# Kernel optimization log

Measured on AMD Instinct MI355X. Metric: run time of the kernel, lower is better.

Reference implementation:

```python
import jax, jax.numpy as jnp
import numpy as np

HOP = jnp.array([0, 1, 4, 7, 2, 5, 8, 3, 6, 9, 11, 14, 10, 12, 15, 13, 16])
GRAPH = jnp.array([0, 1, 4, 7, 2, 5, 8, 3, 6, 9, 12, 10, 13, 15, 11, 14, 16])
D_MODEL, L, D_INNER, D_STATE, DT_RANK = 512, 17, 1024, 4, 32


def layernorm(x, w, b, eps=1e-5):
    mu = x.mean(-1, keepdims=True)
    var = ((x - mu) ** 2).mean(-1, keepdims=True)
    return (x - mu) * jax.lax.rsqrt(var + eps) * w + b


def setup_inputs() -> dict:
    key = jax.random.key(0)
    ks = jax.random.split(key, 9)
    B = 4096
    s = lambda k, shape: jax.random.normal(k, shape, jnp.float32) * 0.02
    # A_log init per mamba_ssm: log(1..d_state) repeated over d_inner
    A_log = jnp.log(jnp.broadcast_to(jnp.arange(1, D_STATE + 1, dtype=jnp.float32), (D_INNER, D_STATE)))
    return {
        "x": jax.random.normal(ks[0], (B, L, D_MODEL), jnp.float32),
        "bp_embed": s(ks[1], (1, 5, D_MODEL)),
        "ln_w": jnp.ones((D_MODEL,), jnp.float32),
        "ln_b": jnp.zeros((D_MODEL,), jnp.float32),
        "in_proj_w": s(ks[2], (2 * D_INNER, D_MODEL)),
        "conv_w": 1.0 + s(ks[3], (D_INNER,)),  # d_conv=1 depthwise conv == per-channel scale
        "conv_b": jnp.zeros((D_INNER,), jnp.float32),
        "x_proj_w": s(ks[4], (DT_RANK + 2 * D_STATE, D_INNER)),
        "dt_proj_w": s(ks[5], (D_INNER, DT_RANK)),
        "dt_proj_b": s(ks[6], (D_INNER,)) - 4.0,  # softplus-inverse-ish small dt init
        "A_log": A_log,
        "D": jnp.ones((D_INNER,), jnp.float32),
        "out_proj_w": s(ks[7], (D_MODEL, D_INNER)),
    }


def mamba(u, in_proj_w, conv_w, conv_b, x_proj_w, dt_proj_w, dt_proj_b, A_log, D, out_proj_w):
    # u: [B, L, d_model]
    xz = jnp.einsum('bld,ed->ble', u, in_proj_w)          # [B,L,2*d_inner]
    xm, z = jnp.split(xz, 2, axis=-1)
    xm = jax.nn.silu(xm * conv_w + conv_b)                 # d_conv=1 -> pointwise
    x_dbl = jnp.einsum('ble,fe->blf', xm, x_proj_w)        # [B,L,dt_rank+2*d_state]
    dt_r = x_dbl[..., :DT_RANK]
    Bm = x_dbl[..., DT_RANK:DT_RANK + D_STATE]
    Cm = x_dbl[..., DT_RANK + D_STATE:]
    dt = jax.nn.softplus(jnp.einsum('blr,er->ble', dt_r, dt_proj_w) + dt_proj_b)  # [B,L,d_inner]
    A = -jnp.exp(A_log)                                    # [d_inner,d_state]

    def step(h, inp):
        dt_t, B_t, C_t, x_t = inp                          # [B,di],[B,ds],[B,ds],[B,di]
        dA = jnp.exp(dt_t[..., None] * A)                  # [B,di,ds]
        h = dA * h + (dt_t * x_t)[..., None] * B_t[:, None, :]
        y = jnp.einsum('bes,bs->be', h, C_t)
        return h, y

    bsz = u.shape[0]
    h0 = jnp.zeros((bsz, D_INNER, D_STATE), u.dtype)
    seq = (dt.transpose(1, 0, 2), Bm.transpose(1, 0, 2), Cm.transpose(1, 0, 2), xm.transpose(1, 0, 2))
    _, ys = jax.lax.scan(step, h0, seq)                    # ys: [L,B,d_inner]
    y = ys.transpose(1, 0, 2) + xm * D
    y = y * jax.nn.silu(z)
    return jnp.einsum('ble,de->bld', y, out_proj_w)


def reference(x, bp_embed, ln_w, ln_b, in_proj_w, conv_w, conv_b, x_proj_w,
              dt_proj_w, dt_proj_b, A_log, D, out_proj_w):
    bp = bp_embed
    x_bpe = jnp.concatenate([bp[:, :3], bp[:, :3], bp[:, :3], bp[:, :1],
                             bp[:, 3:], bp[:, :1], bp[:, 3:], bp[:, 3:]], axis=1)  # [1,17,dim]
    x_ssm = x[:, HOP, :] + x_bpe
    x_ssm = layernorm(x_ssm, ln_w, ln_b)
    x_ssm = mamba(x_ssm, in_proj_w, conv_w, conv_b, x_proj_w,
                  dt_proj_w, dt_proj_b, A_log, D, out_proj_w)
    return x + x_ssm[:, GRAPH, :]
```

## Files before the change

### kernel.cpp

```cpp
#include <hip/hip_runtime.h>

typedef unsigned short u16;
typedef unsigned int   u32;
typedef __bf16 bf16_t;
typedef bf16_t bf16x8 __attribute__((ext_vector_type(8)));
typedef float  f32x4  __attribute__((ext_vector_type(4)));

#define DEV static __device__ __forceinline__

__constant__ int c_HOP[17] = {0,1,4,7,2,5,8,3,6,9,11,14,10,12,15,13,16};
__constant__ int c_BPE[17] = {0,1,2,0,1,2,0,1,2,0,3,4,0,3,4,3,4};

DEV u16 f2bf(float f){
  u32 x = __builtin_bit_cast(u32, f);
  x += 0x7fffu + ((x >> 16) & 1u);
  return (u16)(x >> 16);
}
DEV float bf2f(u32 u){ return __builtin_bit_cast(float, u << 16); }
DEV float silu_f(float v){ return v / (1.f + __expf(-v)); }
DEV float softplus_f(float s){ return (s > 20.f) ? s : log1pf(__expf(s)); }

DEV void gll16(const void* g, void* l){
  __builtin_amdgcn_global_load_lds((__attribute__((address_space(1))) void*)g,
                                   (__attribute__((address_space(3))) void*)l,
                                   16, 0, 0);
}

__global__ __launch_bounds__(256) void cvt4(
    const float* __restrict__ s0, u16* __restrict__ d0, int n0,
    const float* __restrict__ s1, u16* __restrict__ d1, int n1,
    const float* __restrict__ s2, u16* __restrict__ d2, int n2,
    const float* __restrict__ s3, u16* __restrict__ d3, int n3)
{
  int t = blockIdx.x * 256 + threadIdx.x;
  if (t < n0){ d0[t] = f2bf(s0[t]); return; }
  t -= n0; if (t < n1){ d1[t] = f2bf(s1[t]); return; }
  t -= n1; if (t < n2){ d2[t] = f2bf(s2[t]); return; }
  t -= n2; if (t < n3){ d3[t] = f2bf(s3[t]); }
}

__global__ __launch_bounds__(256) void ln_gather(
    const float* __restrict__ x, const float* __restrict__ bpe,
    const float* __restrict__ lnw, const float* __restrict__ lnb,
    u16* __restrict__ u)
{
  int tok = blockIdx.x;
  int b = tok / 17;
  int l = tok - b * 17;
  const float* xr = x   + ((size_t)b * 17 + c_HOP[l]) * 512;
  const float* br = bpe + (size_t)c_BPE[l] * 512;
  int tid = threadIdx.x;
  int d0 = tid * 2;
  float2 xv = *(const float2*)(xr + d0);
  float2 bv = *(const float2*)(br + d0);
  float v0 = xv.x + bv.x, v1 = xv.y + bv.y;

  __shared__ float red[8];
  float s = v0 + v1;
  #pragma unroll
  for (int o = 32; o; o >>= 1) s += __shfl_xor(s, o);
  if ((tid & 63) == 0) red[tid >> 6] = s;
  __syncthreads();
  float mu = (red[0] + red[1] + red[2] + red[3]) * (1.f / 512.f);
  float a0 = v0 - mu, a1 = v1 - mu;
  float q = a0 * a0 + a1 * a1;
  #pragma unroll
  for (int o = 32; o; o >>= 1) q += __shfl_xor(q, o);
  if ((tid & 63) == 0) red[4 + (tid >> 6)] = q;
  __syncthreads();
  float var = (red[4] + red[5] + red[6] + red[7]) * (1.f / 512.f);
  float rs = rsqrtf(var + 1e-5f);

  u16 o0 = f2bf(a0 * rs * lnw[d0]     + lnb[d0]);
  u16 o1 = f2bf(a1 * rs * lnw[d0 + 1] + lnb[d0 + 1]);
  u32 pack = (u32)o0 | ((u32)o1 << 16);
  *(u32*)(u + (size_t)tok * 512 + d0) = pack;
}

enum { EPI_SPLIT = 0, EPI_OUT = 1, EPI_XDBL = 2, EPI_DT = 3 };

template<int EPI>
__global__ __launch_bounds__(512, 2) void gemm256(
    const u16* __restrict__ A, int lda,
    const u16* __restrict__ W, int K, int MT,
    u16* __restrict__ ob0, u16* __restrict__ ob1,
    const float* __restrict__ p0, const float* __restrict__ p1,
    const float* __restrict__ xres, float* __restrict__ fout)
{
  __shared__ u16 sA[2][2][8192];
  __shared__ u16 sB[2][2][8192];

  int nwg = gridDim.x;
  int cpx = nwg >> 3;
  int wg = (blockIdx.x & 7) * cpx + (blockIdx.x >> 3);
  int NT = nwg / MT;
  int nt = wg % NT, mt = wg / NT;
  int brow = mt * 256, bcol = nt * 256;
  int tid = threadIdx.x, lane = tid & 63, wid = tid >> 6;
  int wm = wid >> 2, wn = wid & 3;
  int l15 = lane & 15, lhi = lane >> 4;

  f32x4 acc[8][4] = {};

  int sr0 = tid >> 2, sr1 = 128 + (tid >> 2), sch = tid & 3;
  const u16* gA0 = A + (size_t)(brow + sr0) * lda + (sch ^ ((sr0 >> 1) & 3)) * 8;
  const u16* gA1 = A + (size_t)(brow + sr1) * lda + (sch ^ ((sr1 >> 1) & 3)) * 8;
  const u16* gW0 = W + (size_t)(bcol + sr0) * K   + (sch ^ ((sr0 >> 1) & 3)) * 8;
  const u16* gW1 = W + (size_t)(bcol + sr1) * K   + (sch ^ ((sr1 >> 1) & 3)) * 8;

  auto stA = [&](int buf, int kh, int koff) {
    char* d = (char*)&sA[buf][kh][0] + tid * 16;
    gll16(gA0 + koff, d);
    gll16(gA1 + koff, d + 8192);
  };
  auto stB = [&](int buf, int kh, int koff) {
    char* d = (char*)&sB[buf][kh][0] + tid * 16;
    gll16(gW0 + koff, d);
    gll16(gW1 + koff, d + 8192);
  };

  int aoff[2][4], boff[4];
  #pragma unroll
  for (int mh = 0; mh < 2; mh++)
    #pragma unroll
    for (int mi = 0; mi < 4; mi++) {
      int r = wm * 128 + mh * 64 + mi * 16 + l15;
      aoff[mh][mi] = r * 64 + ((lhi ^ ((r >> 1) & 3)) * 16);
    }
  #pragma unroll
  for (int ni = 0; ni < 4; ni++) {
    int r = wn * 64 + ni * 16 + l15;
    boff[ni] = r * 64 + ((lhi ^ ((r >> 1) & 3)) * 16);
  }

  bf16x8 bvv[4];

#define PH(buf, kh, MH, RB, STAGE)                                          \
  {                                                                         \
    const char* la = (const char*)&sA[buf][kh][0];                          \
    bf16x8 av0 = *(const bf16x8*)(la + aoff[MH][0]);                        \
    bf16x8 av1 = *(const bf16x8*)(la + aoff[MH][1]);                        \
    bf16x8 av2 = *(const bf16x8*)(la + aoff[MH][2]);                        \
    bf16x8 av3 = *(const bf16x8*)(la + aoff[MH][3]);                        \
    if (RB) {                                                               \
      const char* lb = (const char*)&sB[buf][kh][0];                        \
      bvv[0] = *(const bf16x8*)(lb + boff[0]);                              \
      bvv[1] = *(const bf16x8*)(lb + boff[1]);                              \
      bvv[2] = *(const bf16x8*)(lb + boff[2]);                              \
      bvv[3] = *(const bf16x8*)(lb + boff[3]);                              \
    }                                                                       \
    STAGE                                                                   \
    __builtin_amdgcn_s_barrier();                                           \
    __builtin_amdgcn_sched_barrier(0);                                      \
    __builtin_amdgcn_s_setprio(1);                                          \
    _Pragma("unroll")                                                       \
    for (int ni = 0; ni < 4; ni++) {                                        \
      acc[(MH)*4+0][ni] = __builtin_amdgcn_mfma_f32_16x16x32_bf16(av0, bvv[ni], acc[(MH)*4+0][ni], 0,0,0); \
      acc[(MH)*4+1][ni] = __builtin_amdgcn_mfma_f32_16x16x32_bf16(av1, bvv[ni], acc[(MH)*4+1][ni], 0,0,0); \
      acc[(MH)*4+2][ni] = __builtin_amdgcn_mfma_f32_16x16x32_bf16(av2, bvv[ni], acc[(MH)*4+2][ni], 0,0,0); \
      acc[(MH)*4+3][ni] = __builtin_amdgcn_mfma_f32_16x16x32_bf16(av3, bvv[ni], acc[(MH)*4+3][ni], 0,0,0); \
    }                                                                       \
    __builtin_amdgcn_s_setprio(0);                                          \
  }

  int T = K >> 6;

  stA(0, 0, 0);  stB(0, 0, 0);
  stA(0, 1, 32); stB(0, 1, 32);
  stA(1, 0, 64); stB(1, 0, 64);
  asm volatile("s_waitcnt vmcnt(8)" ::: "memory");
  __builtin_amdgcn_s_barrier();

  for (int t = 0; t < T; ++t) {
    int b = t & 1;
    bool s1 = (t + 1 < T), s2 = (t + 2 < T);
    int k1off = ((t + 1) << 6) + 32;
    int k2off = (t + 2) << 6;

    PH(b, 0, 0, true,  { if (s1) stA(b ^ 1, 1, k1off); });
    __builtin_amdgcn_s_barrier();
    PH(b, 0, 1, false, { if (s1) stB(b ^ 1, 1, k1off); });
    if (t < T - 1) { asm volatile("s_waitcnt vmcnt(8)" ::: "memory"); }
    else           { asm volatile("s_waitcnt vmcnt(0)" ::: "memory"); }
    __builtin_amdgcn_s_barrier();
    PH(b, 1, 0, true,  { if (s2) stA(b, 0, k2off); });
    __builtin_amdgcn_s_barrier();
    PH(b, 1, 1, false, { if (s2) stB(b, 0, k2off); });
    if (t < T - 2)       { asm volatile("s_waitcnt vmcnt(8)" ::: "memory"); }
    else if (t == T - 2) { asm volatile("s_waitcnt vmcnt(4)" ::: "memory"); }
    __builtin_amdgcn_s_barrier();
  }
#undef PH

  int r4 = lhi * 4;
  #pragma unroll
  for (int fm = 0; fm < 8; fm++) {
    int rowb = brow + wm * 128 + fm * 16 + r4;
    #pragma unroll
    for (int ni = 0; ni < 4; ni++) {
      int col = bcol + wn * 64 + ni * 16 + l15;
      if constexpr (EPI == EPI_SPLIT) {
        bool isx = (bcol < 1024);
        int cidx = isx ? col : 0;
        float cw = isx ? p0[cidx] : 1.f;
        float cb = isx ? p1[cidx] : 0.f;
        u16* dst = isx ? (ob0 + col) : (ob1 + col - 1024);
        #pragma unroll
        for (int rr = 0; rr < 4; rr++)
          dst[(size_t)(rowb + rr) * 1024] = f2bf(silu_f(acc[fm][ni][rr] * cw + cb));
      } else {
        #pragma unroll
        for (int rr = 0; rr < 4; rr++) {
          int row = rowb + rr;
          u32 rw = (u32)row;
          u32 b = rw / 17u;
          int gl = (int)(rw - b * 17u);
          size_t oi = ((size_t)b * 17 + c_HOP[gl]) * 512 + col;
          fout[oi] = xres[oi] + acc[fm][ni][rr];
        }
      }
    }
  }
}

template<int EPI>
__global__ __launch_bounds__(256) void gemm_bt(
    const u16* __restrict__ A, int lda,
    const u16* __restrict__ W, int K, int MT,
    u16* __restrict__ ob0, const float* __restrict__ p0)
{
  __shared__ u16 sA[2][128 * 32];
  __shared__ u16 sW[2][128 * 32];
  int nwg = gridDim.x;
  int cpx = nwg >> 3;
  int wg = (blockIdx.x & 7) * cpx + (blockIdx.x >> 3);
  int NT = nwg / MT;
  int nt = wg % NT, mt = wg / NT;
  int brow = mt * 128, bcol = nt * 128;
  int tid = threadIdx.x, lane = tid & 63, wid = tid >> 6;
  int wm = wid >> 1, wn = wid & 1;

  f32x4 acc[4][4] = {};

  int srow = tid >> 2;
  int sch  = tid & 3;

  const u16* gA0 = A + (size_t)(brow + srow)      * lda + (sch ^ ((srow >> 1) & 3)) * 8;
  const u16* gA1 = A + (size_t)(brow + 64 + srow) * lda + (sch ^ (((64 + srow) >> 1) & 3)) * 8;
  const u16* gW0 = W + (size_t)(bcol + srow)      * K   + (sch ^ ((srow >> 1) & 3)) * 8;
  const u16* gW1 = W + (size_t)(bcol + 64 + srow) * K   + (sch ^ (((64 + srow) >> 1) & 3)) * 8;

  auto STAGE = [&](int buf, int kt) {
    gll16(gA0 + kt, (char*)sA[buf] + tid * 16);
    gll16(gA1 + kt, (char*)sA[buf] + tid * 16 + 4096);
    gll16(gW0 + kt, (char*)sW[buf] + tid * 16);
    gll16(gW1 + kt, (char*)sW[buf] + tid * 16 + 4096);
  };

  int aoff[4], boff[4];
  #pragma unroll
  for (int mi = 0; mi < 4; mi++) {
    int r = wm * 64 + mi * 16 + (lane & 15);
    aoff[mi] = r * 64 + (((lane >> 4) ^ ((r >> 1) & 3)) * 16);
  }
  #pragma unroll
  for (int ni = 0; ni < 4; ni++) {
    int r = wn * 64 + ni * 16 + (lane & 15);
    boff[ni] = r * 64 + (((lane >> 4) ^ ((r >> 1) & 3)) * 16);
  }

  auto COMPUTE = [&](int buf) {
    bf16x8 av[4], bv[4];
    #pragma unroll
    for (int mi = 0; mi < 4; mi++)
      av[mi] = *(const bf16x8*)((const char*)sA[buf] + aoff[mi]);
    #pragma unroll
    for (int ni = 0; ni < 4; ni++)
      bv[ni] = *(const bf16x8*)((const char*)sW[buf] + boff[ni]);
    #pragma unroll
    for (int mi = 0; mi < 4; mi++)
      #pragma unroll
      for (int ni = 0; ni < 4; ni++)
        acc[mi][ni] = __builtin_amdgcn_mfma_f32_16x16x32_bf16(
            av[mi], bv[ni], acc[mi][ni], 0, 0, 0);
  };

  int nsteps = K >> 5;
  STAGE(0, 0);
  __syncthreads();
  int cur = 0;
  for (int s = 1; s < nsteps; ++s) {
    STAGE(cur ^ 1, s << 5);
    COMPUTE(cur);
    __syncthreads();
    cur ^= 1;
  }
  COMPUTE(cur);

  int r4 = (lane >> 4) * 4;
  int cl = lane & 15;
  #pragma unroll
  for (int mi = 0; mi < 4; mi++) {
    int rowb = brow + wm * 64 + mi * 16 + r4;
    #pragma unroll
    for (int ni = 0; ni < 4; ni++) {
      int col = bcol + wn * 64 + ni * 16 + cl;
      if constexpr (EPI == EPI_XDBL) {
        if (col < 40) {
          #pragma unroll
          for (int rr = 0; rr < 4; rr++)
            ob0[(size_t)(rowb + rr) * 40 + col] = f2bf(acc[mi][ni][rr]);
        }
      } else {
        float bb = p0[col];
        #pragma unroll
        for (int rr = 0; rr < 4; rr++)
          ob0[(size_t)(rowb + rr) * 1024 + col] = f2bf(softplus_f(acc[mi][ni][rr] + bb));
      }
    }
  }
}

__global__ __launch_bounds__(128) void scan5(
    const u16* __restrict__ xm, const u16* __restrict__ zs,
    const u16* __restrict__ xdbl, u16* __restrict__ dty,
    const float* __restrict__ A_log, const float* __restrict__ Dp)
{
  int b = blockIdx.x;
  int tid = threadIdx.x;
  int e0 = tid * 8;
  const size_t base = (size_t)b * 17 * 1024;

  float4 al = *(const float4*)(A_log + (size_t)e0 * 4);
  float A0 = -__expf(al.x), A1 = -__expf(al.y);
  float A2 = -__expf(al.z), A3 = -__expf(al.w);
  float Dv[8];
  *(float4*)(Dv)     = *(const float4*)(Dp + e0);
  *(float4*)(Dv + 4) = *(const float4*)(Dp + e0 + 4);

  const u16* xmb = xm + base + e0;
  const u16* zsb = zs + base + e0;
  u16* db = dty + base + e0;
  const u16* bcb = xdbl + (size_t)b * 680 + 32;

  float h[8][4];
  #pragma unroll
  for (int c = 0; c < 8; c++)
    #pragma unroll
    for (int s = 0; s < 4; s++) h[c][s] = 0.f;

  #pragma unroll
  for (int t = 0; t < 17; t++) {
    uint4 xr = *(const uint4*)(xmb + t * 1024);
    uint4 zr = *(const uint4*)(zsb + t * 1024);
    uint4 dr = *(const uint4*)(db + t * 1024);
    uint4 bc = *(const uint4*)(bcb + t * 40);
    float B0 = bf2f(bc.x & 0xffffu), B1 = bf2f(bc.x >> 16);
    float B2 = bf2f(bc.y & 0xffffu), B3 = bf2f(bc.y >> 16);
    float C0 = bf2f(bc.z & 0xffffu), C1 = bf2f(bc.z >> 16);
    float C2 = bf2f(bc.w & 0xffffu), C3 = bf2f(bc.w >> 16);
    u32 yo[4];
    const u32* xw = (const u32*)&xr;
    const u32* zw = (const u32*)&zr;
    const u32* dw = (const u32*)&dr;
    #pragma unroll
    for (int c = 0; c < 8; c++) {
      u32 x16 = (c & 1) ? (xw[c >> 1] >> 16) : (xw[c >> 1] & 0xffffu);
      u32 z16 = (c & 1) ? (zw[c >> 1] >> 16) : (zw[c >> 1] & 0xffffu);
      u32 d16 = (c & 1) ? (dw[c >> 1] >> 16) : (dw[c >> 1] & 0xffffu);
      float xv = bf2f(x16), zv = bf2f(z16), dtv = bf2f(d16);
      float dx = dtv * xv;
      h[c][0] = __expf(dtv * A0) * h[c][0] + dx * B0;
      h[c][1] = __expf(dtv * A1) * h[c][1] + dx * B1;
      h[c][2] = __expf(dtv * A2) * h[c][2] + dx * B2;
      h[c][3] = __expf(dtv * A3) * h[c][3] + dx * B3;
      float yv = h[c][0] * C0 + h[c][1] * C1 + h[c][2] * C2 + h[c][3] * C3;
      u16 pk = f2bf((yv + xv * Dv[c]) * zv);
      if (c & 1) yo[c >> 1] |= ((u32)pk << 16);
      else       yo[c >> 1] = (u32)pk;
    }
    *(uint4*)(db + t * 1024) = *(uint4*)yo;
  }
}

extern "C" void kernel_launch(void* const* d_in, const int* in_sizes, int n_in,
                              void* d_out, int out_size, void* d_ws, size_t ws_size,
                              hipStream_t stream) {
  const float* x     = (const float*)d_in[0];
  const float* bpe   = (const float*)d_in[1];
  const float* lnw   = (const float*)d_in[2];
  const float* lnb   = (const float*)d_in[3];
  const float* w_in  = (const float*)d_in[4];
  const float* convw = (const float*)d_in[5];
  const float* convb = (const float*)d_in[6];
  const float* w_xp  = (const float*)d_in[7];
  const float* w_dt  = (const float*)d_in[8];
  const float* b_dt  = (const float*)d_in[9];
  const float* A_log = (const float*)d_in[10];
  const float* Dp    = (const float*)d_in[11];
  const float* w_out = (const float*)d_in[12];
  float* out = (float*)d_out;

  u16* ws = (u16*)d_ws;
  u16* wb_in  = ws;
  u16* wb_out = wb_in  + 1048576;
  u16* wb_xp  = wb_out + 524288;
  u16* wb_dt  = wb_xp  + 40960;
  u16* xm     = wb_dt  + 32768;
  u16* zs     = xm     + 71303168;
  u16* xdbl   = zs     + 71303168;
  u16* dty    = xdbl   + 2785280;
  u16* u      = dty;

  const int MT2 = 272;
  const int MT1 = 544;

  cvt4<<<6432, 256, 0, stream>>>(w_in, wb_in, 1048576, w_out, wb_out, 524288,
                                 w_xp, wb_xp, 40960, w_dt, wb_dt, 32768);

  ln_gather<<<69632, 256, 0, stream>>>(x, bpe, lnw, lnb, u);

  gemm256<EPI_SPLIT><<<MT2 * 8, 512, 0, stream>>>(
      u, 512, wb_in, 512, MT2, xm, zs, convw, convb, nullptr, nullptr);

  gemm_bt<EPI_XDBL><<<MT1 * 1, 256, 0, stream>>>(
      xm, 1024, wb_xp, 1024, MT1, xdbl, nullptr);

  gemm_bt<EPI_DT><<<MT1 * 8, 256, 0, stream>>>(
      xdbl, 40, wb_dt, 32, MT1, dty, b_dt);

  scan5<<<4096, 128, 0, stream>>>(xm, zs, xdbl, dty, A_log, Dp);

  gemm256<EPI_OUT><<<MT2 * 2, 512, 0, stream>>>(
      dty, 1024, wb_out, 1024, MT2, nullptr, nullptr, nullptr, nullptr, x, out);
}
```

Measured before the change: 872.0 us.

## Fuse x_proj and dt_proj GEMMs into one kernel and restructure gemm256 main loop

Merges the x_proj GEMM and the dt_proj GEMM with softplus into a single kernel. The 32-wide dt_rank slice stays in shared memory and feeds a second small MFMA stage, so there is no separate launch and no global round trip for that slice. Separately, the gemm256 inner loop now issues the A and B loads for each half-step together, then runs 32 MFMAs per half in place of four phases with extra barriers. The x_proj weight rows are clamped to row 39 to avoid out-of-bounds reads, which adds some redundant staging. The fused kernel's dt epilogue has only 544 blocks doing scattered 2-byte stores, which could limit parallelism.

```diff
diff --git a/kernel.cpp b/kernel.cpp
--- a/kernel.cpp
+++ b/kernel.cpp
@@ -77,7 +77,7 @@
   *(u32*)(u + (size_t)tok * 512 + d0) = pack;
 }
 
-enum { EPI_SPLIT = 0, EPI_OUT = 1, EPI_XDBL = 2, EPI_DT = 3 };
+enum { EPI_SPLIT = 0, EPI_OUT = 1 };
 
 template<int EPI>
 __global__ __launch_bounds__(512, 2) void gemm256(
@@ -133,34 +133,56 @@
     boff[ni] = r * 64 + ((lhi ^ ((r >> 1) & 3)) * 16);
   }
 
-  bf16x8 bvv[4];
-
-#define PH(buf, kh, MH, RB, STAGE)                                          \
-  {                                                                         \
-    const char* la = (const char*)&sA[buf][kh][0];                          \
-    bf16x8 av0 = *(const bf16x8*)(la + aoff[MH][0]);                        \
-    bf16x8 av1 = *(const bf16x8*)(la + aoff[MH][1]);                        \
-    bf16x8 av2 = *(const bf16x8*)(la + aoff[MH][2]);                        \
-    bf16x8 av3 = *(const bf16x8*)(la + aoff[MH][3]);                        \
-    if (RB) {                                                               \
-      const char* lb = (const char*)&sB[buf][kh][0];                        \
-      bvv[0] = *(const bf16x8*)(lb + boff[0]);                              \
-      bvv[1] = *(const bf16x8*)(lb + boff[1]);                              \
-      bvv[2] = *(const bf16x8*)(lb + boff[2]);                              \
-      bvv[3] = *(const bf16x8*)(lb + boff[3]);                              \
-    }                                                                       \
-    STAGE                                                                   \
-    __builtin_amdgcn_s_barrier();                                           \
-    __builtin_amdgcn_sched_barrier(0);                                      \
-    __builtin_amdgcn_s_setprio(1);                                          \
-    _Pragma("unroll")                                                       \
-    for (int ni = 0; ni < 4; ni++) {                                        \
-      acc[(MH)*4+0][ni] = __builtin_amdgcn_mfma_f32_16x16x32_bf16(av0, bvv[ni], acc[(MH)*4+0][ni], 0,0,0); \
-      acc[(MH)*4+1][ni] = __builtin_amdgcn_mfma_f32_16x16x32_bf16(av1, bvv[ni], acc[(MH)*4+1][ni], 0,0,0); \
-      acc[(MH)*4+2][ni] = __builtin_amdgcn_mfma_f32_16x16x32_bf16(av2, bvv[ni], acc[(MH)*4+2][ni], 0,0,0); \
-      acc[(MH)*4+3][ni] = __builtin_amdgcn_mfma_f32_16x16x32_bf16(av3, bvv[ni], acc[(MH)*4+3][ni], 0,0,0); \
-    }                                                                       \
-    __builtin_amdgcn_s_setprio(0);                                          \
+#define HALF(BUF, KH)                                                        \
+  {                                                                          \
+    const char* la = (const char*)&sA[BUF][KH][0];                           \
+    const char* lb = (const char*)&sB[BUF][KH][0];                           \
+    bf16x8 bv0 = *(const bf16x8*)(lb + boff[0]);                             \
+    bf16x8 bv1 = *(const bf16x8*)(lb + boff[1]);                             \
+    bf16x8 bv2 = *(const bf16x8*)(lb + boff[2]);                             \
+    bf16x8 bv3 = *(const bf16x8*)(lb + boff[3]);                             \
+    bf16x8 a0 = *(const bf16x8*)(la + aoff[0][0]);                           \
+    bf16x8 a1 = *(const bf16x8*)(la + aoff[0][1]);                           \
+    bf16x8 a2 = *(const bf16x8*)(la + aoff[0][2]);                           \
+    bf16x8 a3 = *(const bf16x8*)(la + aoff[0][3]);                           \
+    __builtin_amdgcn_s_setprio(1);                                           \
+    acc[0][0] = __builtin_amdgcn_mfma_f32_16x16x32_bf16(a0, bv0, acc[0][0],0,0,0); \
+    acc[1][0] = __builtin_amdgcn_mfma_f32_16x16x32_bf16(a1, bv0, acc[1][0],0,0,0); \
+    acc[2][0] = __builtin_amdgcn_mfma_f32_16x16x32_bf16(a2, bv0, acc[2][0],0,0,0); \
+    acc[3][0] = __builtin_amdgcn_mfma_f32_16x16x32_bf16(a3, bv0, acc[3][0],0,0,0); \
+    acc[0][1] = __builtin_amdgcn_mfma_f32_16x16x32_bf16(a0, bv1, acc[0][1],0,0,0); \
+    acc[1][1] = __builtin_amdgcn_mfma_f32_16x16x32_bf16(a1, bv1, acc[1][1],0,0,0); \
+    acc[2][1] = __builtin_amdgcn_mfma_f32_16x16x32_bf16(a2, bv1, acc[2][1],0,0,0); \
+    acc[3][1] = __builtin_amdgcn_mfma_f32_16x16x32_bf16(a3, bv1, acc[3][1],0,0,0); \
+    acc[0][2] = __builtin_amdgcn_mfma_f32_16x16x32_bf16(a0, bv2, acc[0][2],0,0,0); \
+    acc[1][2] = __builtin_amdgcn_mfma_f32_16x16x32_bf16(a1, bv2, acc[1][2],0,0,0); \
+    acc[2][2] = __builtin_amdgcn_mfma_f32_16x16x32_bf16(a2, bv2, acc[2][2],0,0,0); \
+    acc[3][2] = __builtin_amdgcn_mfma_f32_16x16x32_bf16(a3, bv2, acc[3][2],0,0,0); \
+    acc[0][3] = __builtin_amdgcn_mfma_f32_16x16x32_bf16(a0, bv3, acc[0][3],0,0,0); \
+    acc[1][3] = __builtin_amdgcn_mfma_f32_16x16x32_bf16(a1, bv3, acc[1][3],0,0,0); \
+    acc[2][3] = __builtin_amdgcn_mfma_f32_16x16x32_bf16(a2, bv3, acc[2][3],0,0,0); \
+    acc[3][3] = __builtin_amdgcn_mfma_f32_16x16x32_bf16(a3, bv3, acc[3][3],0,0,0); \
+    a0 = *(const bf16x8*)(la + aoff[1][0]);                                  \
+    a1 = *(const bf16x8*)(la + aoff[1][1]);                                  \
+    a2 = *(const bf16x8*)(la + aoff[1][2]);                                  \
+    a3 = *(const bf16x8*)(la + aoff[1][3]);                                  \
+    acc[4][0] = __builtin_amdgcn_mfma_f32_16x16x32_bf16(a0, bv0, acc[4][0],0,0,0); \
+    acc[5][0] = __builtin_amdgcn_mfma_f32_16x16x32_bf16(a1, bv0, acc[5][0],0,0,0); \
+    acc[6][0] = __builtin_amdgcn_mfma_f32_16x16x32_bf16(a2, bv0, acc[6][0],0,0,0); \
+    acc[7][0] = __builtin_amdgcn_mfma_f32_16x16x32_bf16(a3, bv0, acc[7][0],0,0,0); \
+    acc[4][1] = __builtin_amdgcn_mfma_f32_16x16x32_bf16(a0, bv1, acc[4][1],0,0,0); \
+    acc[5][1] = __builtin_amdgcn_mfma_f32_16x16x32_bf16(a1, bv1, acc[5][1],0,0,0); \
+    acc[6][1] = __builtin_amdgcn_mfma_f32_16x16x32_bf16(a2, bv1, acc[6][1],0,0,0); \
+    acc[7][1] = __builtin_amdgcn_mfma_f32_16x16x32_bf16(a3, bv1, acc[7][1],0,0,0); \
+    acc[4][2] = __builtin_amdgcn_mfma_f32_16x16x32_bf16(a0, bv2, acc[4][2],0,0,0); \
+    acc[5][2] = __builtin_amdgcn_mfma_f32_16x16x32_bf16(a1, bv2, acc[5][2],0,0,0); \
+    acc[6][2] = __builtin_amdgcn_mfma_f32_16x16x32_bf16(a2, bv2, acc[6][2],0,0,0); \
+    acc[7][2] = __builtin_amdgcn_mfma_f32_16x16x32_bf16(a3, bv2, acc[7][2],0,0,0); \
+    acc[4][3] = __builtin_amdgcn_mfma_f32_16x16x32_bf16(a0, bv3, acc[4][3],0,0,0); \
+    acc[5][3] = __builtin_amdgcn_mfma_f32_16x16x32_bf16(a1, bv3, acc[5][3],0,0,0); \
+    acc[6][3] = __builtin_amdgcn_mfma_f32_16x16x32_bf16(a2, bv3, acc[6][3],0,0,0); \
+    acc[7][3] = __builtin_amdgcn_mfma_f32_16x16x32_bf16(a3, bv3, acc[7][3],0,0,0); \
+    __builtin_amdgcn_s_setprio(0);                                           \
   }
 
   int T = K >> 6;
@@ -170,27 +192,25 @@
   stA(1, 0, 64); stB(1, 0, 64);
   asm volatile("s_waitcnt vmcnt(8)" ::: "memory");
   __builtin_amdgcn_s_barrier();
+  __builtin_amdgcn_sched_barrier(0);
 
   for (int t = 0; t < T; ++t) {
-    int b = t & 1;
-    bool s1 = (t + 1 < T), s2 = (t + 2 < T);
-    int k1off = ((t + 1) << 6) + 32;
-    int k2off = (t + 2) << 6;
-
-    PH(b, 0, 0, true,  { if (s1) stA(b ^ 1, 1, k1off); });
-    __builtin_amdgcn_s_barrier();
-    PH(b, 0, 1, false, { if (s1) stB(b ^ 1, 1, k1off); });
+    int bb_ = t & 1;
+    if (t + 1 < T) { int ko = ((t + 1) << 6) + 32; stA(bb_ ^ 1, 1, ko); stB(bb_ ^ 1, 1, ko); }
+    HALF(bb_, 0);
     if (t < T - 1) { asm volatile("s_waitcnt vmcnt(8)" ::: "memory"); }
     else           { asm volatile("s_waitcnt vmcnt(0)" ::: "memory"); }
     __builtin_amdgcn_s_barrier();
-    PH(b, 1, 0, true,  { if (s2) stA(b, 0, k2off); });
+    __builtin_amdgcn_sched_barrier(0);
+    if (t + 2 < T) { int ko = (t + 2) << 6; stA(bb_, 0, ko); stB(bb_, 0, ko); }
+    HALF(bb_, 1);
+    if (t < T - 2)      { asm volatile("s_waitcnt vmcnt(8)" ::: "memory"); }
+    else if (t == T - 2){ asm volatile("s_waitcnt vmcnt(4)" ::: "memory"); }
+    else                { asm volatile("s_waitcnt vmcnt(0)" ::: "memory"); }
     __builtin_amdgcn_s_barrier();
-    PH(b, 1, 1, false, { if (s2) stB(b, 0, k2off); });
-    if (t < T - 2)       { asm volatile("s_waitcnt vmcnt(8)" ::: "memory"); }
-    else if (t == T - 2) { asm volatile("s_waitcnt vmcnt(4)" ::: "memory"); }
-    __builtin_amdgcn_s_barrier();
-  }
-#undef PH
+    __builtin_amdgcn_sched_barrier(0);
+  }
+#undef HALF
 
   int r4 = lhi * 4;
   #pragma unroll
@@ -223,32 +243,38 @@
   }
 }
 
-template<int EPI>
-__global__ __launch_bounds__(256) void gemm_bt(
-    const u16* __restrict__ A, int lda,
-    const u16* __restrict__ W, int K, int MT,
-    u16* __restrict__ ob0, const float* __restrict__ p0)
+__global__ __launch_bounds__(256) void xproj_dt(
+    const u16* __restrict__ A,
+    const u16* __restrict__ Wx,
+    const u16* __restrict__ wdt,
+    const float* __restrict__ bdt,
+    u16* __restrict__ xdbl, u16* __restrict__ dty, int MT)
 {
   __shared__ u16 sA[2][128 * 32];
   __shared__ u16 sW[2][128 * 32];
+  __shared__ u16 x2s[128][40];
+
   int nwg = gridDim.x;
   int cpx = nwg >> 3;
   int wg = (blockIdx.x & 7) * cpx + (blockIdx.x >> 3);
-  int NT = nwg / MT;
-  int nt = wg % NT, mt = wg / NT;
-  int brow = mt * 128, bcol = nt * 128;
+  int mt = wg;
+  int brow = mt * 128;
   int tid = threadIdx.x, lane = tid & 63, wid = tid >> 6;
   int wm = wid >> 1, wn = wid & 1;
+  int l15 = lane & 15, lhi = lane >> 4;
+  const int K = 1024;
 
   f32x4 acc[4][4] = {};
 
   int srow = tid >> 2;
   int sch  = tid & 3;
 
-  const u16* gA0 = A + (size_t)(brow + srow)      * lda + (sch ^ ((srow >> 1) & 3)) * 8;
-  const u16* gA1 = A + (size_t)(brow + 64 + srow) * lda + (sch ^ (((64 + srow) >> 1) & 3)) * 8;
-  const u16* gW0 = W + (size_t)(bcol + srow)      * K   + (sch ^ ((srow >> 1) & 3)) * 8;
-  const u16* gW1 = W + (size_t)(bcol + 64 + srow) * K   + (sch ^ (((64 + srow) >> 1) & 3)) * 8;
+  const u16* gA0 = A + (size_t)(brow + srow)      * K + (sch ^ ((srow >> 1) & 3)) * 8;
+  const u16* gA1 = A + (size_t)(brow + 64 + srow) * K + (sch ^ (((64 + srow) >> 1) & 3)) * 8;
+  int wr0 = srow < 40 ? srow : 39;
+  int wr1 = 39;
+  const u16* gW0 = Wx + (size_t)wr0 * K + (sch ^ ((srow >> 1) & 3)) * 8;
+  const u16* gW1 = Wx + (size_t)wr1 * K + (sch ^ (((64 + srow) >> 1) & 3)) * 8;
 
   auto STAGE = [&](int buf, int kt) {
     gll16(gA0 + kt, (char*)sA[buf] + tid * 16);
@@ -260,13 +286,13 @@
   int aoff[4], boff[4];
   #pragma unroll
   for (int mi = 0; mi < 4; mi++) {
-    int r = wm * 64 + mi * 16 + (lane & 15);
-    aoff[mi] = r * 64 + (((lane >> 4) ^ ((r >> 1) & 3)) * 16);
+    int r = wm * 64 + mi * 16 + l15;
+    aoff[mi] = r * 64 + (((lhi) ^ ((r >> 1) & 3)) * 16);
   }
   #pragma unroll
   for (int ni = 0; ni < 4; ni++) {
-    int r = wn * 64 + ni * 16 + (lane & 15);
-    boff[ni] = r * 64 + (((lane >> 4) ^ ((r >> 1) & 3)) * 16);
+    int r = wn * 64 + ni * 16 + l15;
+    boff[ni] = r * 64 + (((lhi) ^ ((r >> 1) & 3)) * 16);
   }
 
   auto COMPUTE = [&](int buf) {
@@ -297,25 +323,42 @@
   }
   COMPUTE(cur);
 
-  int r4 = (lane >> 4) * 4;
-  int cl = lane & 15;
+  int r4 = lhi * 4;
   #pragma unroll
   for (int mi = 0; mi < 4; mi++) {
-    int rowb = brow + wm * 64 + mi * 16 + r4;
+    int rowb = wm * 64 + mi * 16 + r4;
     #pragma unroll
     for (int ni = 0; ni < 4; ni++) {
-      int col = bcol + wn * 64 + ni * 16 + cl;
-      if constexpr (EPI == EPI_XDBL) {
-        if (col < 40) {
-          #pragma unroll
-          for (int rr = 0; rr < 4; rr++)
-            ob0[(size_t)(rowb + rr) * 40 + col] = f2bf(acc[mi][ni][rr]);
+      int col = wn * 64 + ni * 16 + l15;
+      if (col < 40) {
+        #pragma unroll
+        for (int rr = 0; rr < 4; rr++) {
+          u16 v = f2bf(acc[mi][ni][rr]);
+          xdbl[(size_t)(brow + rowb + rr) * 40 + col] = v;
+          if (col < 32) x2s[rowb + rr][col] = v;
         }
-      } else {
-        float bb = p0[col];
-        #pragma unroll
-        for (int rr = 0; rr < 4; rr++)
-          ob0[(size_t)(rowb + rr) * 1024 + col] = f2bf(softplus_f(acc[mi][ni][rr] + bb));
+      }
+    }
+  }
+  __syncthreads();
+
+  bf16x8 a2[8];
+  #pragma unroll
+  for (int mf = 0; mf < 8; mf++)
+    a2[mf] = *(const bf16x8*)(&x2s[mf * 16 + l15][lhi * 8]);
+  #pragma unroll
+  for (int cf = 0; cf < 16; cf++) {
+    int e = wid * 256 + cf * 16 + l15;
+    bf16x8 bv = *(const bf16x8*)(wdt + (size_t)e * 32 + lhi * 8);
+    float bb = bdt[e];
+    #pragma unroll
+    for (int mf = 0; mf < 8; mf++) {
+      f32x4 c2 = {};
+      c2 = __builtin_amdgcn_mfma_f32_16x16x32_bf16(a2[mf], bv, c2, 0, 0, 0);
+      #pragma unroll
+      for (int rr = 0; rr < 4; rr++) {
+        int row = brow + mf * 16 + lhi * 4 + rr;
+        dty[(size_t)row * 1024 + e] = f2bf(softplus_f(c2[rr] + bb));
       }
     }
   }
@@ -423,11 +466,8 @@
   gemm256<EPI_SPLIT><<<MT2 * 8, 512, 0, stream>>>(
       u, 512, wb_in, 512, MT2, xm, zs, convw, convb, nullptr, nullptr);
 
-  gemm_bt<EPI_XDBL><<<MT1 * 1, 256, 0, stream>>>(
-      xm, 1024, wb_xp, 1024, MT1, xdbl, nullptr);
-
-  gemm_bt<EPI_DT><<<MT1 * 8, 256, 0, stream>>>(
-      xdbl, 40, wb_dt, 32, MT1, dty, b_dt);
+  xproj_dt<<<MT1, 256, 0, stream>>>(
+      xm, wb_xp, wb_dt, b_dt, xdbl, dty, MT1);
 
   scan5<<<4096, 128, 0, stream>>>(xm, zs, xdbl, dty, A_log, Dp);
 
```

Result: slower. 1.158 ms (+32.7%).
